# Optimization experiments

Measured on AMD Instinct MI355X. Metric: run time of the kernel, lower is better.

Reference implementation:

```python
import jax, jax.numpy as jnp
import numpy as np

NUM_EMBEDDINGS = 8192
EMBEDDING_DIM = 512
COMMITMENT_COST = 0.25
BATCH = 32768


def setup_inputs() -> dict:
    key = jax.random.key(0)
    k_in, k_cb = jax.random.split(key)
    inputs = jax.random.normal(k_in, (BATCH, EMBEDDING_DIM), dtype=jnp.float32)
    # xavier_uniform_ on [num_embeddings, embedding_dim]
    limit = float(np.sqrt(6.0 / (NUM_EMBEDDINGS + EMBEDDING_DIM)))
    codebook = jax.random.uniform(k_cb, (NUM_EMBEDDINGS, EMBEDDING_DIM),
                                  dtype=jnp.float32, minval=-limit, maxval=limit)
    return {"inputs": inputs, "codebook": codebook}


def reference(inputs, codebook):
    # distances[b, n] = ||x_b||^2 + ||e_n||^2 - 2 x_b . e_n  (cdist^2 via matmul)
    distances = (jnp.sum(inputs ** 2, axis=1, keepdims=True)
                 + jnp.sum(codebook ** 2, axis=1)
                 - 2.0 * jnp.matmul(inputs, codebook.T))
    encoding_indices = jnp.argmin(distances, axis=1)  # [B]

    # one-hot @ codebook is just a row gather
    quantized = codebook[encoding_indices]  # [B, D]

    e_latent_loss = jnp.mean((jax.lax.stop_gradient(quantized) - inputs) ** 2)
    q_latent_loss = jnp.mean((quantized - jax.lax.stop_gradient(inputs)) ** 2)
    loss = q_latent_loss + COMMITMENT_COST * e_latent_loss

    # straight-through estimator
    quantized_st = inputs + jax.lax.stop_gradient(quantized - inputs)

    # avg_probs = mean over batch of one-hot encodings -> normalized bincount
    counts = jnp.zeros((NUM_EMBEDDINGS,), dtype=jnp.float32).at[encoding_indices].add(1.0)
    avg_probs = counts / BATCH
    perplexity = jnp.exp(-jnp.sum(avg_probs * jnp.log(avg_probs + 1e-10)))

    return quantized_st, loss, perplexity
```

## Files before the change

### kernel.cpp

```cpp
#include <hip/hip_runtime.h>
#include <math.h>

#define BATCH 32768
#define D 512
#define NE 8192
#define NSPLIT 4
#define ESPAN (NE / NSPLIT)
#define NT 64
#define KC 128
#define MARGIN 1.6e-2f

typedef float    f32x4 __attribute__((ext_vector_type(4)));
typedef _Float16 f16x8 __attribute__((ext_vector_type(8)));

__device__ __forceinline__ void g2l16(const void* g, void* l) {
    __builtin_amdgcn_global_load_lds((const __attribute__((address_space(1))) void*)g,
                                     (__attribute__((address_space(3))) void*)l, 16, 0, 0);
}
__device__ __forceinline__ unsigned short f2h(float f) {
    union { _Float16 h; unsigned short u; } c; c.h = (_Float16)f; return c.u;
}

__global__ void vq_norms_kernel(const float* __restrict__ cb, float* __restrict__ norms) {
    int row  = blockIdx.x * 4 + (threadIdx.x >> 6);
    int lane = threadIdx.x & 63;
    const float4* p = (const float4*)(cb + (size_t)row * D);
    float s = 0.f;
#pragma unroll
    for (int i = 0; i < 2; ++i) {
        float4 v = p[lane + 64 * i];
        s += v.x * v.x + v.y * v.y + v.z * v.z + v.w * v.w;
    }
    for (int off = 32; off; off >>= 1) s += __shfl_down(s, off);
    if (lane == 0) norms[row] = s;
}

__global__ void vq_cvt_swz(const float* __restrict__ cb, unsigned short* __restrict__ eq) {
    int i = blockIdx.x * 256 + threadIdx.x;
    int n = i >> 6, g = i & 63;
    int ch = g >> 4;
    int sl = (g & 15) ^ (n & 15);
    const float4* sp = (const float4*)(cb + (size_t)n * D + g * 8);
    float4 a = sp[0], b = sp[1];
    ushort4* dp = (ushort4*)(eq + (size_t)n * D + ch * KC + sl * 8);
    dp[0] = make_ushort4(f2h(a.x), f2h(a.y), f2h(a.z), f2h(a.w));
    dp[1] = make_ushort4(f2h(b.x), f2h(b.y), f2h(b.z), f2h(b.w));
}

__global__ __launch_bounds__(512, 2)
void vq_topk2(const float* __restrict__ x, const unsigned short* __restrict__ eq,
              const float* __restrict__ norms, float4* __restrict__ cands) {
    __shared__ unsigned short es[2][NT * KC];

    const int t = threadIdx.x;
    const int w = t >> 6, lane = t & 63, l15 = lane & 15, l4 = lane >> 4;
    const int b = blockIdx.x;
    const int xcd = b & 7;
    const int sp  = xcd >> 1;
    const int rb  = ((xcd & 1) << 6) | (b >> 3);
    const size_t row0 = (size_t)rb * 256;
    const int nbase = sp * ESPAN;

    f16x8 af[2][16];
#pragma unroll
    for (int mi = 0; mi < 2; ++mi) {
        const float4* xp = (const float4*)(x + (row0 + w * 32 + mi * 16 + l15) * D);
#pragma unroll
        for (int ks = 0; ks < 16; ++ks) {
            float4 p0 = xp[ks * 8 + l4 * 2];
            float4 p1 = xp[ks * 8 + l4 * 2 + 1];
            f16x8 v;
            v[0] = (_Float16)p0.x; v[1] = (_Float16)p0.y;
            v[2] = (_Float16)p0.z; v[3] = (_Float16)p0.w;
            v[4] = (_Float16)p1.x; v[5] = (_Float16)p1.y;
            v[6] = (_Float16)p1.z; v[7] = (_Float16)p1.w;
            af[mi][ks] = v;
        }
    }

    float v1[8], v2[8];
    int   i1[8], i2[8];
#pragma unroll
    for (int s = 0; s < 8; ++s) { v1[s] = v2[s] = 3.4e38f; i1[s] = i2[s] = 0x7fffffff; }

#define STAGE(BUFI, STEP) do {                                                          \
        const int snt_ = (STEP) >> 2, sch_ = (STEP) & 3;                                \
        const int nb_ = nbase + snt_ * NT;                                              \
        _Pragma("unroll")                                                               \
        for (int i_ = 0; i_ < 2; ++i_) {                                                \
            int c_ = i_ * 512 + t;                                                      \
            int row_ = c_ >> 4, sl_ = c_ & 15;                                          \
            g2l16(eq + (size_t)(nb_ + row_) * D + sch_ * KC + sl_ * 8,                  \
                  &es[BUFI][(i_ * 512 + w * 64) * 8]);                                  \
        }                                                                               \
    } while (0)

    STAGE(0, 0);
    __syncthreads();
    int buf = 0;

    for (int nt = 0; nt < ESPAN / NT; ++nt) {
        const int n0 = nbase + nt * NT;
        f32x4 acc[2][4];
#pragma unroll
        for (int mi = 0; mi < 2; ++mi)
#pragma unroll
            for (int ni = 0; ni < 4; ++ni) acc[mi][ni] = (f32x4){0.f, 0.f, 0.f, 0.f};

#pragma unroll
        for (int ch = 0; ch < 4; ++ch) {
            const int step = nt * 4 + ch + 1;
            if (step < (ESPAN / NT) * 4) STAGE(buf ^ 1, step);
            const char* esp = (const char*)es[buf];
#pragma unroll
            for (int ksb = 0; ksb < 4; ++ksb) {
                f16x8 bfr[4];
#pragma unroll
                for (int ni = 0; ni < 4; ++ni) {
                    int slot = ((ksb << 2) | l4) ^ l15;
                    bfr[ni] = *(const f16x8*)(esp + ni * 4096 + l15 * 256 + slot * 16);
                }
#pragma unroll
                for (int mi = 0; mi < 2; ++mi)
#pragma unroll
                    for (int ni = 0; ni < 4; ++ni)
                        acc[mi][ni] = __builtin_amdgcn_mfma_f32_16x16x32_f16(
                            af[mi][ch * 4 + ksb], bfr[ni], acc[mi][ni], 0, 0, 0);
            }
            __syncthreads();
            buf ^= 1;
        }

        float nn[4];
#pragma unroll
        for (int ni = 0; ni < 4; ++ni) nn[ni] = norms[n0 + ni * 16 + l15];
#pragma unroll
        for (int mi = 0; mi < 2; ++mi)
#pragma unroll
            for (int r = 0; r < 4; ++r) {
                int s = mi * 4 + r;
#pragma unroll
                for (int ni = 0; ni < 4; ++ni) {
                    float dd = fmaf(-2.f, acc[mi][ni][r], nn[ni]);
                    int   cc = n0 + ni * 16 + l15;
                    if (dd < v2[s]) {
                        bool b1 = dd < v1[s];
                        v2[s] = b1 ? v1[s] : dd; i2[s] = b1 ? i1[s] : cc;
                        v1[s] = b1 ? dd : v1[s]; i1[s] = b1 ? cc : i1[s];
                    }
                }
            }
    }
#undef STAGE

#pragma unroll
    for (int s = 0; s < 8; ++s) {
        int mi = s >> 2, r = s & 3;
        size_t rowc = row0 + w * 32 + mi * 16 + l4 * 4 + r;
        cands[rowc * 64 + sp * 16 + l15] =
            make_float4(v1[s], __int_as_float(i1[s]), v2[s], __int_as_float(i2[s]));
    }
}

__global__ __launch_bounds__(512)
void vq_finish(const float* __restrict__ x, const float* __restrict__ cb,
               const float* __restrict__ norms, const float4* __restrict__ cands,
               float* __restrict__ counts, float* __restrict__ psum, float* __restrict__ out) {
    __shared__ float red[8];
    const int t = threadIdx.x, w = t >> 6, lane = t & 63;
    const size_t row = (size_t)blockIdx.x * 8 + w;

    float4 c4 = cands[row * 64 + lane];
    float va = c4.x, vb = c4.z;
    int   ia = __float_as_int(c4.y), ib = __float_as_int(c4.w);
    float m = fminf(va, vb);
#pragma unroll
    for (int off = 1; off < 64; off <<= 1) m = fminf(m, __shfl_xor(m, off));
    const float thr = m + MARGIN;

    const float4* xp = (const float4*)(x + row * D);
    float4 xa = xp[lane * 2], xb = xp[lane * 2 + 1];

    float bd = 3.4e38f; int bi = 0x7fffffff;
#pragma unroll 1
    for (int q = 0; q < 2; ++q) {
        unsigned long long mk = __ballot((q == 0 ? va : vb) <= thr);
        while (mk) {
            int src = __builtin_ctzll(mk);
            mk &= mk - 1;
            int ci = __shfl(q == 0 ? ia : ib, src);
            const float4* ep = (const float4*)(cb + (size_t)ci * D);
            float4 ea = ep[lane * 2], eb = ep[lane * 2 + 1];
            float s = 0.f;
            s = fmaf(xa.x, ea.x, s); s = fmaf(xa.y, ea.y, s);
            s = fmaf(xa.z, ea.z, s); s = fmaf(xa.w, ea.w, s);
            s = fmaf(xb.x, eb.x, s); s = fmaf(xb.y, eb.y, s);
            s = fmaf(xb.z, eb.z, s); s = fmaf(xb.w, eb.w, s);
#pragma unroll
            for (int off = 1; off < 64; off <<= 1) s += __shfl_xor(s, off);
            float dd = fmaf(-2.f, s, norms[ci]);
            if (dd < bd || (dd == bd && ci < bi)) { bd = dd; bi = ci; }
        }
    }

    const float4* qp = (const float4*)(cb + (size_t)bi * D);
    float4 qa = qp[lane * 2], qb = qp[lane * 2 + 1];
    float4* op = (float4*)(out + row * D);
    float s2 = 0.f;
    float4 oa, ob;
    {
        float d0 = qa.x - xa.x; oa.x = xa.x + d0; s2 = fmaf(d0, d0, s2);
        float d1 = qa.y - xa.y; oa.y = xa.y + d1; s2 = fmaf(d1, d1, s2);
        float d2 = qa.z - xa.z; oa.z = xa.z + d2; s2 = fmaf(d2, d2, s2);
        float d3 = qa.w - xa.w; oa.w = xa.w + d3; s2 = fmaf(d3, d3, s2);
        float d4 = qb.x - xb.x; ob.x = xb.x + d4; s2 = fmaf(d4, d4, s2);
        float d5 = qb.y - xb.y; ob.y = xb.y + d5; s2 = fmaf(d5, d5, s2);
        float d6 = qb.z - xb.z; ob.z = xb.z + d6; s2 = fmaf(d6, d6, s2);
        float d7 = qb.w - xb.w; ob.w = xb.w + d7; s2 = fmaf(d7, d7, s2);
    }
    op[lane * 2] = oa; op[lane * 2 + 1] = ob;
    for (int off = 32; off; off >>= 1) s2 += __shfl_down(s2, off);
    if (lane == 0) {
        red[w] = s2;
        atomicAdd(&counts[bi], 1.0f);
    }
    __syncthreads();
    if (t == 0) {
        float s = 0.f;
#pragma unroll
        for (int i = 0; i < 8; ++i) s += red[i];
        psum[blockIdx.x] = s;
    }
}

__global__ void vq_finalize_kernel(const float* __restrict__ counts, const float* __restrict__ psum,
                                   float* __restrict__ out2) {
    __shared__ float rede[256];
    __shared__ float reds[256];
    float se = 0.f, ss = 0.f;
    for (int i = threadIdx.x; i < NE; i += 256) {
        float p = counts[i] * (1.0f / (float)BATCH);
        se += p * logf(p + 1e-10f);
    }
    for (int i = threadIdx.x; i < 4096; i += 256) ss += psum[i];
    rede[threadIdx.x] = se; reds[threadIdx.x] = ss;
    __syncthreads();
    for (int off = 128; off; off >>= 1) {
        if (threadIdx.x < off) {
            rede[threadIdx.x] += rede[threadIdx.x + off];
            reds[threadIdx.x] += reds[threadIdx.x + off];
        }
        __syncthreads();
    }
    if (threadIdx.x == 0) {
        out2[0] = 1.25f * reds[0] * (1.0f / (float)((size_t)BATCH * D));
        out2[1] = expf(-rede[0]);
    }
}

#define BM 64
#define BN 64
#define BK 16
#define LDSP 68
__global__ __launch_bounds__(256)
void vq_argmin_kernel(const float* __restrict__ x, const float* __restrict__ cb,
                      const float* __restrict__ norms, int* __restrict__ out_idx) {
    __shared__ float xs[BK * LDSP];
    __shared__ float es[BK * LDSP];
    __shared__ float rv[BM][16];
    __shared__ int   ri[BM][16];
    const int t = threadIdx.x, tx = t & 15, ty = t >> 4;
    const int row0 = blockIdx.x * BM, ldrow = t >> 2, ldq = t & 3;
    float minv[4]; int mini[4];
#pragma unroll
    for (int i = 0; i < 4; ++i) { minv[i] = 3.4e38f; mini[i] = 0; }
    for (int n0 = 0; n0 < NE; n0 += BN) {
        float acc[4][4];
#pragma unroll
        for (int i = 0; i < 4; ++i)
#pragma unroll
            for (int j = 0; j < 4; ++j) acc[i][j] = 0.f;
        for (int kk = 0; kk < D; kk += BK) {
            __syncthreads();
            float4 xv = *(const float4*)&x [(size_t)(row0 + ldrow) * D + kk + ldq * 4];
            float4 ev = *(const float4*)&cb[(size_t)(n0   + ldrow) * D + kk + ldq * 4];
            const float* xvp = (const float*)&xv;
            const float* evp = (const float*)&ev;
#pragma unroll
            for (int j = 0; j < 4; ++j) {
                xs[(ldq * 4 + j) * LDSP + ldrow] = xvp[j];
                es[(ldq * 4 + j) * LDSP + ldrow] = evp[j];
            }
            __syncthreads();
#pragma unroll
            for (int k = 0; k < BK; ++k) {
                float4 xr4 = *(const float4*)&xs[k * LDSP + ty * 4];
                float4 er4 = *(const float4*)&es[k * LDSP + tx * 4];
                const float xr[4] = {xr4.x, xr4.y, xr4.z, xr4.w};
                const float er[4] = {er4.x, er4.y, er4.z, er4.w};
#pragma unroll
                for (int i = 0; i < 4; ++i)
#pragma unroll
                    for (int j = 0; j < 4; ++j)
                        acc[i][j] = fmaf(xr[i], er[j], acc[i][j]);
            }
        }
#pragma unroll
        for (int j = 0; j < 4; ++j) {
            int n = n0 + tx * 4 + j;
            float nnv = norms[n];
#pragma unroll
            for (int i = 0; i < 4; ++i) {
                float dd = fmaf(-2.f, acc[i][j], nnv);
                if (dd < minv[i]) { minv[i] = dd; mini[i] = n; }
            }
        }
    }
    __syncthreads();
#pragma unroll
    for (int i = 0; i < 4; ++i) { rv[ty * 4 + i][tx] = minv[i]; ri[ty * 4 + i][tx] = mini[i]; }
    __syncthreads();
    if (t < BM) {
        float bv = rv[t][0]; int bi = ri[t][0];
#pragma unroll
        for (int j = 1; j < 16; ++j) {
            float v = rv[t][j]; int iz = ri[t][j];
            if (v < bv || (v == bv && iz < bi)) { bv = v; bi = iz; }
        }
        out_idx[row0 + t] = bi;
    }
}

__global__ void vq_gather_kernel(const float* __restrict__ x, const float* __restrict__ cb,
                                 const int* __restrict__ idx, float* __restrict__ out,
                                 float* __restrict__ counts, float* __restrict__ psum) {
    const int b = blockIdx.x, lane = threadIdx.x;
    const int e = idx[b];
    const float4* xp = (const float4*)(x  + (size_t)b * D);
    const float4* qp = (const float4*)(cb + (size_t)e * D);
    float4*       op = (float4*)(out + (size_t)b * D);
    float s = 0.f;
#pragma unroll
    for (int i = 0; i < 2; ++i) {
        float4 xv = xp[lane + 64 * i];
        float4 qv = qp[lane + 64 * i];
        float4 ov;
        float dx = qv.x - xv.x; ov.x = xv.x + dx; s = fmaf(dx, dx, s);
        float dy = qv.y - xv.y; ov.y = xv.y + dy; s = fmaf(dy, dy, s);
        float dz = qv.z - xv.z; ov.z = xv.z + dz; s = fmaf(dz, dz, s);
        float dw = qv.w - xv.w; ov.w = xv.w + dw; s = fmaf(dw, dw, s);
        op[lane + 64 * i] = ov;
    }
    for (int off = 32; off; off >>= 1) s += __shfl_down(s, off);
    if (lane == 0) {
        atomicAdd(&psum[0], s);
        atomicAdd(&counts[e], 1.0f);
    }
}

extern "C" void kernel_launch(void* const* d_in, const int* in_sizes, int n_in,
                              void* d_out, int out_size, void* d_ws, size_t ws_size,
                              hipStream_t stream) {
    const float* x  = (const float*)d_in[0];
    const float* cb = (const float*)d_in[1];
    float* out = (float*)d_out;

    char* ws = (char*)d_ws;
    float*  norms  = (float*)ws;
    float*  counts = (float*)(ws + 32768);
    float*  psum   = (float*)(ws + 65536);
    int*    idx    = (int*)(ws + 81920);
    float4* cands  = (float4*)(ws + 262144);
    unsigned short* eq = (unsigned short*)(ws + 33816576);
    const size_t WS_NEED = 42205184;

    hipMemsetAsync(counts, 0, NE * sizeof(float), stream);
    vq_norms_kernel<<<NE / 4, 256, 0, stream>>>(cb, norms);

    if (ws_size >= WS_NEED) {
        vq_cvt_swz<<<NE * 64 / 256, 256, 0, stream>>>(cb, eq);
        vq_topk2<<<512, 512, 0, stream>>>(x, eq, norms, cands);
        vq_finish<<<BATCH / 8, 512, 0, stream>>>(x, cb, norms, cands, counts, psum, out);
    } else {
        hipMemsetAsync(psum, 0, 4096 * sizeof(float), stream);
        vq_argmin_kernel<<<BATCH / BM, 256, 0, stream>>>(x, cb, norms, idx);
        vq_gather_kernel<<<BATCH, 64, 0, stream>>>(x, cb, idx, out, counts, psum);
    }
    vq_finalize_kernel<<<1, 256, 0, stream>>>(counts, psum, out + (size_t)BATCH * D);
}
```

Baseline: 443.5 us.

## Shrink topk blocks to 256 threads and restructure codebook staging pipeline

The top-2 distance kernel now uses 256-thread blocks covering 128 rows each, with twice as many blocks. The staging loop issues the next chunk's loads right after a single waitcnt+barrier, so only one barrier is paid per chunk instead of two. Wave priority is raised around the MFMA section. The split's codebook norms are preloaded into LDS once rather than read from global memory each tile. Halving the rows per block doubles the codebook traffic per row, and the code after the cut must still index rows consistently with the new mapping.

After: 424.8 us. -4.2%, faster.

```diff
diff --git a/kernel.cpp b/kernel.cpp
--- a/kernel.cpp
+++ b/kernel.cpp
@@ -8,6 +8,7 @@
 #define ESPAN (NE / NSPLIT)
 #define NT 64
 #define KC 128
+#define NPHASE ((ESPAN / NT) * 4)
 #define MARGIN 1.6e-2f
 
 typedef float    f32x4 __attribute__((ext_vector_type(4)));
@@ -47,19 +48,40 @@
     dp[1] = make_ushort4(f2h(b.x), f2h(b.y), f2h(b.z), f2h(b.w));
 }
 
-__global__ __launch_bounds__(512, 2)
+__global__ __launch_bounds__(256, 2)
 void vq_topk2(const float* __restrict__ x, const unsigned short* __restrict__ eq,
               const float* __restrict__ norms, float4* __restrict__ cands) {
-    __shared__ unsigned short es[2][NT * KC];
+    __shared__ char arena[40960];
+    unsigned short* es0 = (unsigned short*)arena;
+    unsigned short* es1 = (unsigned short*)(arena + 16384);
+    float*          nlds = (float*)(arena + 32768);
 
     const int t = threadIdx.x;
     const int w = t >> 6, lane = t & 63, l15 = lane & 15, l4 = lane >> 4;
     const int b = blockIdx.x;
     const int xcd = b & 7;
     const int sp  = xcd >> 1;
-    const int rb  = ((xcd & 1) << 6) | (b >> 3);
-    const size_t row0 = (size_t)rb * 256;
+    const int rb  = ((b >> 3) << 1) | (xcd & 1);
+    const size_t row0 = (size_t)rb * 128;
     const int nbase = sp * ESPAN;
+
+#define STAGE(DST, STEP) do {                                                           \
+        const int snt_ = (STEP) >> 2, sch_ = (STEP) & 3;                                \
+        _Pragma("unroll")                                                               \
+        for (int i_ = 0; i_ < 4; ++i_) {                                                \
+            int c_ = i_ * 256 + t;                                                      \
+            int row_ = c_ >> 4, sl_ = c_ & 15;                                          \
+            g2l16(eq + (size_t)(nbase + snt_ * NT + row_) * D + sch_ * KC + sl_ * 8,    \
+                  (DST) + (size_t)(i_ * 256 + w * 64) * 8);                             \
+        }                                                                               \
+    } while (0)
+
+    STAGE(es0, 0);
+#pragma unroll
+    for (int i = 0; i < 2; ++i) {
+        int c = i * 256 + t;
+        g2l16(norms + nbase + c * 4, (char*)nlds + (size_t)(i * 256 + w * 64) * 16);
+    }
 
     f16x8 af[2][16];
 #pragma unroll
@@ -83,24 +105,10 @@
 #pragma unroll
     for (int s = 0; s < 8; ++s) { v1[s] = v2[s] = 3.4e38f; i1[s] = i2[s] = 0x7fffffff; }
 
-#define STAGE(BUFI, STEP) do {                                                          \
-        const int snt_ = (STEP) >> 2, sch_ = (STEP) & 3;                                \
-        const int nb_ = nbase + snt_ * NT;                                              \
-        _Pragma("unroll")                                                               \
-        for (int i_ = 0; i_ < 2; ++i_) {                                                \
-            int c_ = i_ * 512 + t;                                                      \
-            int row_ = c_ >> 4, sl_ = c_ & 15;                                          \
-            g2l16(eq + (size_t)(nb_ + row_) * D + sch_ * KC + sl_ * 8,                  \
-                  &es[BUFI][(i_ * 512 + w * 64) * 8]);                                  \
-        }                                                                               \
-    } while (0)
-
-    STAGE(0, 0);
-    __syncthreads();
-    int buf = 0;
-
-    for (int nt = 0; nt < ESPAN / NT; ++nt) {
-        const int n0 = nbase + nt * NT;
+    unsigned short* cur = es0;
+    unsigned short* nxt = es1;
+
+    for (int nt_ = 0; nt_ < ESPAN / NT; ++nt_) {
         f32x4 acc[2][4];
 #pragma unroll
         for (int mi = 0; mi < 2; ++mi)
@@ -109,16 +117,19 @@
 
 #pragma unroll
         for (int ch = 0; ch < 4; ++ch) {
-            const int step = nt * 4 + ch + 1;
-            if (step < (ESPAN / NT) * 4) STAGE(buf ^ 1, step);
-            const char* esp = (const char*)es[buf];
+            const int step = nt_ * 4 + ch;
+            asm volatile("s_waitcnt vmcnt(0)" ::: "memory");
+            __builtin_amdgcn_s_barrier();
+            __builtin_amdgcn_sched_barrier(0);
+            if (step + 1 < NPHASE) STAGE(nxt, step + 1);
+            __builtin_amdgcn_s_setprio(1);
 #pragma unroll
             for (int ksb = 0; ksb < 4; ++ksb) {
                 f16x8 bfr[4];
 #pragma unroll
                 for (int ni = 0; ni < 4; ++ni) {
                     int slot = ((ksb << 2) | l4) ^ l15;
-                    bfr[ni] = *(const f16x8*)(esp + ni * 4096 + l15 * 256 + slot * 16);
+                    bfr[ni] = *(const f16x8*)((const char*)cur + ni * 4096 + l15 * 256 + slot * 16);
                 }
 #pragma unroll
                 for (int mi = 0; mi < 2; ++mi)
@@ -127,13 +138,14 @@
                         acc[mi][ni] = __builtin_amdgcn_mfma_f32_16x16x32_f16(
                             af[mi][ch * 4 + ksb], bfr[ni], acc[mi][ni], 0, 0, 0);
             }
-            __syncthreads();
-            buf ^= 1;
-        }
-
+            __builtin_amdgcn_s_setprio(0);
+            unsigned short* tswap = cur; cur = nxt; nxt = tswap;
+        }
+
+        const int n0 = nbase + nt_ * NT;
         float nn[4];
 #pragma unroll
-        for (int ni = 0; ni < 4; ++ni) nn[ni] = norms[n0 + ni * 16 + l15];
+        for (int ni = 0; ni < 4; ++ni) nn[ni] = nlds[nt_ * 64 + ni * 16 + l15];
 #pragma unroll
         for (int mi = 0; mi < 2; ++mi)
 #pragma unroll
@@ -379,7 +391,7 @@
 
     if (ws_size >= WS_NEED) {
         vq_cvt_swz<<<NE * 64 / 256, 256, 0, stream>>>(cb, eq);
-        vq_topk2<<<512, 512, 0, stream>>>(x, eq, norms, cands);
+        vq_topk2<<<1024, 256, 0, stream>>>(x, eq, norms, cands);
         vq_finish<<<BATCH / 8, 512, 0, stream>>>(x, cb, norms, cands, counts, psum, out);
     } else {
         hipMemsetAsync(psum, 0, 4096 * sizeof(float), stream);
```
